# Optimization experiments

Measured on AMD Instinct MI355X. Metric: run time of the kernel, lower is better.

The kernel has to match this reference:

```python
import jax, jax.numpy as jnp
import numpy as np

IN_CH = 1024
ATT_DIM = 1024
B, L1, L2 = 8, 2048, 2048


def setup_inputs() -> dict:
    key = jax.random.key(0)
    ks = jax.random.split(key, 8)
    s = 1.0 / np.sqrt(IN_CH)
    return {
        "input_1": jax.random.normal(ks[0], (B, L1, IN_CH), dtype=jnp.float32),
        "input_2": jax.random.normal(ks[1], (B, L2, IN_CH), dtype=jnp.float32),
        "Wq": jax.random.uniform(ks[2], (IN_CH, ATT_DIM), jnp.float32, -s, s),
        "bq": jnp.zeros((ATT_DIM,), jnp.float32),
        "Wk": jax.random.uniform(ks[3], (IN_CH, ATT_DIM), jnp.float32, -s, s),
        "bk": jnp.zeros((ATT_DIM,), jnp.float32),
        "Wv": jax.random.uniform(ks[4], (IN_CH, ATT_DIM), jnp.float32, -s, s),
        "bv": jnp.zeros((ATT_DIM,), jnp.float32),
    }


def reference(input_1, input_2, Wq, bq, Wk, bk, Wv, bv):
    scale = 1.0 / np.sqrt(ATT_DIM).astype(np.float32)
    Q = jnp.einsum("bld,de->ble", input_1, Wq) + bq  # [B, L1, D]
    K = jnp.einsum("bld,de->ble", input_2, Wk) + bk  # [B, L2, D]
    V = jnp.einsum("bld,de->ble", input_2, Wv) + bv  # [B, L2, D]
    scores = jnp.einsum("bqd,bkd->bqk", Q, K) * scale  # [B, L1, L2]
    scores = jnp.clip(scores, -100.0, 100.0)
    weights = jax.nn.softmax(scores, axis=-1)
    return jnp.einsum("bqk,bkd->bqd", weights, V)  # [B, L1, D]
```

## Files before the change

kernel.cpp:

```cpp
#include <hip/hip_runtime.h>
#include <stdint.h>

typedef __attribute__((ext_vector_type(8))) short bf16x8;
typedef __attribute__((ext_vector_type(4))) float f32x4;
typedef __attribute__((ext_vector_type(4))) unsigned short u16x4;
typedef __attribute__((ext_vector_type(8))) unsigned short u16x8;

__device__ __forceinline__ unsigned short f2bf(float f) {
  unsigned int u = __builtin_bit_cast(unsigned int, f);
  u = (u + 0x7fffu + ((u >> 16) & 1u)) >> 16;
  return (unsigned short)u;
}
__device__ __forceinline__ float bf2f(unsigned short s) {
  unsigned int u = ((unsigned int)s) << 16;
  return __builtin_bit_cast(float, u);
}

__device__ __forceinline__ void g2lds16(const void* g, void* l) {
  __builtin_amdgcn_global_load_lds((const __attribute__((address_space(1))) void*)g,
                                   (__attribute__((address_space(3))) void*)l,
                                   16, 0, 0);
}

__global__ __launch_bounds__(256) void cast_f32_bf16(const float* __restrict__ in0,
                                                     unsigned short* __restrict__ out0,
                                                     const float* __restrict__ in1,
                                                     unsigned short* __restrict__ out1,
                                                     int n4) {
  const float* in = blockIdx.z ? in1 : in0;
  unsigned short* out = blockIdx.z ? out1 : out0;
  int i = blockIdx.x * 256 + threadIdx.x;
  const int stride = gridDim.x * 256;
  for (; i < n4; i += stride) {
    float4 v = reinterpret_cast<const float4*>(in)[i];
    u16x4 o;
    o.x = f2bf(v.x); o.y = f2bf(v.y); o.z = f2bf(v.z); o.w = f2bf(v.w);
    reinterpret_cast<u16x4*>(out)[i] = o;
  }
}

__global__ __launch_bounds__(256) void transpose_cast_w(
    const float* __restrict__ W0, const float* __restrict__ W1, const float* __restrict__ W2,
    unsigned short* __restrict__ T0, unsigned short* __restrict__ T1, unsigned short* __restrict__ T2) {
  const float* W = blockIdx.z == 0 ? W0 : (blockIdx.z == 1 ? W1 : W2);
  unsigned short* T = blockIdx.z == 0 ? T0 : (blockIdx.z == 1 ? T1 : T2);
  __shared__ unsigned short tile[32][33];
  const int tx = threadIdx.x & 31, ty = threadIdx.x >> 5;
  const int r0 = blockIdx.y * 32, c0 = blockIdx.x * 32;
#pragma unroll
  for (int i = 0; i < 4; i++) {
    int r = ty + i * 8;
    tile[r][tx] = f2bf(W[(size_t)(r0 + r) * 1024 + c0 + tx]);
  }
  __syncthreads();
#pragma unroll
  for (int i = 0; i < 4; i++) {
    int r = ty + i * 8;
    T[(size_t)(c0 + r) * 1024 + r0 + tx] = tile[tx][r];
  }
}

#define STAGE(buf, ab, h, kt)                                                          \
  {                                                                                    \
    const char* _s = ((ab) ? Bsrc : Asrc) + (size_t)(h) * 128 * K2 + (size_t)(kt) * 128; \
    char* _d = ldsb + (buf) * 65536 + (ab) * 32768 + (h) * 16384 + tid * 16;           \
    g2lds16(_s, _d);                                                                   \
    g2lds16(_s + 64 * K2, _d + 8192);                                                  \
  }
#define LOADA(buf, mh)                                                                 \
  _Pragma("unroll") for (int mf2 = 0; mf2 < 4; mf2++) {                                \
    const char* _p = ldsb + (buf) * 65536 + arow + ((mh) * 128 + mf2 * 16) * 128;      \
    aA[mf2][0] = *(const bf16x8*)(_p + colk0);                                         \
    aA[mf2][1] = *(const bf16x8*)(_p + colk1);                                         \
  }
#define LOADB(buf, nh)                                                                 \
  _Pragma("unroll") for (int nf2 = 0; nf2 < 2; nf2++) {                                \
    const char* _p = ldsb + (buf) * 65536 + 32768 + brow + ((nh) * 128 + nf2 * 16) * 128; \
    bB[nf2][0] = *(const bf16x8*)(_p + colk0);                                         \
    bB[nf2][1] = *(const bf16x8*)(_p + colk1);                                         \
  }
#define MFMAQ(mh, nh)                                                                  \
  __builtin_amdgcn_s_setprio(1);                                                       \
  _Pragma("unroll") for (int mf2 = 0; mf2 < 4; mf2++)                                  \
      _Pragma("unroll") for (int nf2 = 0; nf2 < 2; nf2++) {                            \
    acc[(mh)*4 + mf2][(nh)*2 + nf2] = __builtin_amdgcn_mfma_f32_16x16x32_bf16(         \
        aA[mf2][0], bB[nf2][0], acc[(mh)*4 + mf2][(nh)*2 + nf2], 0, 0, 0);             \
    acc[(mh)*4 + mf2][(nh)*2 + nf2] = __builtin_amdgcn_mfma_f32_16x16x32_bf16(         \
        aA[mf2][1], bB[nf2][1], acc[(mh)*4 + mf2][(nh)*2 + nf2], 0, 0, 0);             \
  }                                                                                    \
  __builtin_amdgcn_s_setprio(0);
#define BAR() __builtin_amdgcn_s_barrier()
#define VMW(n) asm volatile("s_waitcnt vmcnt(" #n ")" ::: "memory")

template <int MODE>
__global__ __launch_bounds__(512, 2) void gemm256(
    const unsigned short* __restrict__ Aall, const unsigned short* __restrict__ Btall,
    const float* __restrict__ bias, void* __restrict__ Call,
    int gm, int gn, int N, int K, long long sA, long long sB, long long sC, float scale) {
  __shared__ unsigned short lds[2][2][16384];

  const int tid = threadIdx.x;
  const int lane = tid & 63;
  const int w = tid >> 6;
  const int wr = w >> 2, wc = w & 3;
  const int lane16 = lane & 15, kg = lane >> 4;

  const int q8 = gridDim.x >> 3;
  const int swz = (blockIdx.x & 7) * q8 + (blockIdx.x >> 3);
  const int z = swz / (gm * gn);
  const int r2 = swz % (gm * gn);
  const int m0 = (r2 / gn) * 256;
  const int n0 = (r2 % gn) * 256;

  const unsigned short* A = Aall + (size_t)z * sA;
  const unsigned short* Bt = Btall + (size_t)z * sB;
  const size_t K2 = (size_t)K * 2;

  const int rowIn = tid >> 3;
  const int colSw = ((tid & 7) * 16) ^ ((rowIn & 7) << 4);
  const char* Asrc = (const char*)A + (size_t)(m0 + rowIn) * K2 + colSw;
  const char* Bsrc = (const char*)Bt + (size_t)(n0 + rowIn) * K2 + colSw;
  char* ldsb = (char*)&lds[0][0][0];

  const int colk0 = ((kg ^ (lane16 & 7)) << 4);
  const int colk1 = colk0 ^ 64;
  const int arow = (wr * 64 + lane16) * 128;
  const int brow = (wc * 32 + lane16) * 128;

  f32x4 acc[8][4] = {};
  bf16x8 aA[4][2], bB[2][2];

  const int nt = K >> 6;
  const int niter = nt >> 1;

  STAGE(0, 0, 0, 0); STAGE(0, 1, 0, 0); STAGE(0, 0, 1, 0); STAGE(0, 1, 1, 0);
  STAGE(1, 0, 0, 1); STAGE(1, 1, 1, 1);
  VMW(4);
  BAR();

  for (int i = 0; i < niter; i++) {
    const int t = 2 * i;
    const bool more = (i + 1 < niter);
    LOADA(0, 0); LOADB(0, 0);
    STAGE(1, 0, 1, t + 1);
    BAR(); MFMAQ(0, 0); BAR();
    LOADB(0, 1);
    STAGE(1, 1, 0, t + 1);
    BAR(); MFMAQ(0, 1); BAR();
    LOADA(0, 1);
    if (more) STAGE(0, 0, 0, t + 2);
    BAR(); MFMAQ(1, 1); BAR();
    LOADB(0, 0);
    if (more) { STAGE(0, 1, 1, t + 2); VMW(4); } else { VMW(0); }
    BAR(); MFMAQ(1, 0); BAR();
    LOADA(1, 0); LOADB(1, 0);
    if (more) STAGE(0, 0, 1, t + 2);
    BAR(); MFMAQ(0, 0); BAR();
    LOADB(1, 1);
    if (more) STAGE(0, 1, 0, t + 2);
    BAR(); MFMAQ(0, 1); BAR();
    LOADA(1, 1);
    if (more) STAGE(1, 0, 0, t + 3);
    BAR(); MFMAQ(1, 1); BAR();
    LOADB(1, 0);
    if (more) { STAGE(1, 1, 1, t + 3); VMW(4); }
    BAR(); MFMAQ(1, 0); BAR();
  }

  const int rb0 = m0 + wr * 64 + kg * 4;
  const int cb0 = n0 + wc * 32 + lane16;
  if constexpr (MODE == 3) {
    float* C = (float*)Call + (size_t)z * sC;
#pragma unroll
    for (int a = 0; a < 8; a++)
#pragma unroll
      for (int j = 0; j < 4; j++) {
        size_t r = (size_t)(rb0 + (a >> 2) * 128 + (a & 3) * 16 + j);
#pragma unroll
        for (int b = 0; b < 4; b++)
          C[r * N + cb0 + (b >> 1) * 128 + (b & 1) * 16] = acc[a][b][j];
      }
  } else {
    unsigned short* C = (unsigned short*)Call + (size_t)z * sC;
    float cb[4] = {0.f, 0.f, 0.f, 0.f};
    if constexpr (MODE == 0) {
#pragma unroll
      for (int b = 0; b < 4; b++) cb[b] = bias[cb0 + (b >> 1) * 128 + (b & 1) * 16];
    }
#pragma unroll
    for (int a = 0; a < 8; a++)
#pragma unroll
      for (int j = 0; j < 4; j++) {
        int r = rb0 + (a >> 2) * 128 + (a & 3) * 16 + j;
        float rbias = 0.0f;
        if constexpr (MODE == 1) rbias = bias[r];
#pragma unroll
        for (int b = 0; b < 4; b++) {
          float v = acc[a][b][j];
          if constexpr (MODE == 0) v += cb[b];
          if constexpr (MODE == 1) v += rbias;
          if constexpr (MODE == 2) {
            v *= scale;
            v = fminf(fmaxf(v, -100.0f), 100.0f);
          }
          C[(size_t)r * N + cb0 + (b >> 1) * 128 + (b & 1) * 16] = f2bf(v);
        }
      }
  }
}

__global__ __launch_bounds__(256) void softmax_rows(unsigned short* __restrict__ S) {
  const size_t row = blockIdx.x;
  unsigned short* p = S + row * 2048;
  const int tid = threadIdx.x;
  const int lane = tid & 63, wv = tid >> 6;

  u16x8 raw = *reinterpret_cast<const u16x8*>(&p[tid * 8]);
  float v[8];
#pragma unroll
  for (int i = 0; i < 8; i++) v[i] = bf2f(raw[i]);

  float m = v[0];
#pragma unroll
  for (int i = 1; i < 8; i++) m = fmaxf(m, v[i]);
#pragma unroll
  for (int off = 32; off > 0; off >>= 1) m = fmaxf(m, __shfl_xor(m, off));

  __shared__ float red[8];
  if (lane == 0) red[wv] = m;
  __syncthreads();
  m = fmaxf(fmaxf(red[0], red[1]), fmaxf(red[2], red[3]));

  float e[8];
  float s = 0.f;
#pragma unroll
  for (int i = 0; i < 8; i++) { e[i] = __expf(v[i] - m); s += e[i]; }
#pragma unroll
  for (int off = 32; off > 0; off >>= 1) s += __shfl_xor(s, off);
  if (lane == 0) red[4 + wv] = s;
  __syncthreads();
  s = red[4] + red[5] + red[6] + red[7];
  const float inv = 1.0f / s;

  u16x8 o;
#pragma unroll
  for (int i = 0; i < 8; i++) o[i] = f2bf(e[i] * inv);
  *reinterpret_cast<u16x8*>(&p[tid * 8]) = o;
}

extern "C" void kernel_launch(void* const* d_in, const int* in_sizes, int n_in,
                              void* d_out, int out_size, void* d_ws, size_t ws_size,
                              hipStream_t stream) {
  const float* X1 = (const float*)d_in[0];
  const float* X2 = (const float*)d_in[1];
  const float* Wq = (const float*)d_in[2];
  const float* bq = (const float*)d_in[3];
  const float* Wk = (const float*)d_in[4];
  const float* bk = (const float*)d_in[5];
  const float* Wv = (const float*)d_in[6];
  const float* bv = (const float*)d_in[7];

  char* ws = (char*)d_ws;
  const size_t MB = 1024 * 1024;
  unsigned short* X1b = (unsigned short*)(ws);
  unsigned short* X2b = (unsigned short*)(ws + 32 * MB);
  unsigned short* Sbuf = (unsigned short*)(ws);
  unsigned short* Wqt = (unsigned short*)(ws + 64 * MB);
  unsigned short* Wkt = (unsigned short*)(ws + 66 * MB);
  unsigned short* Wvt = (unsigned short*)(ws + 68 * MB);
  unsigned short* Vt = (unsigned short*)(ws + 70 * MB);
  unsigned short* Qb = (unsigned short*)d_out;
  unsigned short* Kb = Qb + 16777216;
  float* out = (float*)d_out;

  cast_f32_bf16<<<dim3(2048, 1, 2), 256, 0, stream>>>(X1, X1b, X2, X2b, 4194304);
  transpose_cast_w<<<dim3(32, 32, 3), 256, 0, stream>>>(Wq, Wk, Wv, Wqt, Wkt, Wvt);

  gemm256<0><<<dim3(256), 512, 0, stream>>>(X1b, Wqt, bq, Qb,
                                            64, 4, 1024, 1024, 0, 0, 0, 1.0f);
  gemm256<0><<<dim3(256), 512, 0, stream>>>(X2b, Wkt, bk, Kb,
                                            64, 4, 1024, 1024, 0, 0, 0, 1.0f);
  gemm256<1><<<dim3(256), 512, 0, stream>>>(Wvt, X2b, bv, Vt,
                                            4, 8, 2048, 1024,
                                            0, 2048LL * 1024, 1024LL * 2048, 1.0f);
  gemm256<2><<<dim3(512), 512, 0, stream>>>(Qb, Kb, nullptr, Sbuf,
                                            8, 8, 2048, 1024,
                                            2048LL * 1024, 2048LL * 1024,
                                            2048LL * 2048, 0.03125f);
  softmax_rows<<<16384, 256, 0, stream>>>(Sbuf);
  gemm256<3><<<dim3(256), 512, 0, stream>>>(Sbuf, Vt, nullptr, out,
                                            8, 4, 1024, 2048,
                                            2048LL * 2048, 1024LL * 2048,
                                            2048LL * 1024, 1.0f);
}
```

Baseline: 438.3 us.

## Stage GEMM epilogue through swizzled LDS for coalesced stores; peel last iteration

The GEMM epilogue now writes accumulator tiles into LDS with an XOR swizzle and then writes them out to global memory as 16-byte row-contiguous vectors, replacing the scattered 2-byte and 4-byte stores. The fp32 output mode goes through LDS in two halves because it needs twice the space. The final main-loop iteration is peeled so the per-stage `more` branches disappear. The MFMA order is also changed to issue all k-slice-0 products before the k-slice-1 ones, which spaces out the dependent accumulator updates. In exchange the epilogue gains extra LDS traffic and barriers.

New measurement: 443.7 us. No clear change (+1.2%).

```diff
diff --git a/kernel.cpp b/kernel.cpp
--- a/kernel.cpp
+++ b/kernel.cpp
@@ -81,12 +81,11 @@
   }
 #define MFMAQ(mh, nh)                                                                  \
   __builtin_amdgcn_s_setprio(1);                                                       \
-  _Pragma("unroll") for (int mf2 = 0; mf2 < 4; mf2++)                                  \
-      _Pragma("unroll") for (int nf2 = 0; nf2 < 2; nf2++) {                            \
+  _Pragma("unroll") for (int ks = 0; ks < 2; ks++)                                     \
+      _Pragma("unroll") for (int mf2 = 0; mf2 < 4; mf2++)                              \
+          _Pragma("unroll") for (int nf2 = 0; nf2 < 2; nf2++) {                        \
     acc[(mh)*4 + mf2][(nh)*2 + nf2] = __builtin_amdgcn_mfma_f32_16x16x32_bf16(         \
-        aA[mf2][0], bB[nf2][0], acc[(mh)*4 + mf2][(nh)*2 + nf2], 0, 0, 0);             \
-    acc[(mh)*4 + mf2][(nh)*2 + nf2] = __builtin_amdgcn_mfma_f32_16x16x32_bf16(         \
-        aA[mf2][1], bB[nf2][1], acc[(mh)*4 + mf2][(nh)*2 + nf2], 0, 0, 0);             \
+        aA[mf2][ks], bB[nf2][ks], acc[(mh)*4 + mf2][(nh)*2 + nf2], 0, 0, 0);           \
   }                                                                                    \
   __builtin_amdgcn_s_setprio(0);
 #define BAR() __builtin_amdgcn_s_barrier()
@@ -138,9 +137,8 @@
   VMW(4);
   BAR();
 
-  for (int i = 0; i < niter; i++) {
+  for (int i = 0; i < niter - 1; i++) {
     const int t = 2 * i;
-    const bool more = (i + 1 < niter);
     LOADA(0, 0); LOADB(0, 0);
     STAGE(1, 0, 1, t + 1);
     BAR(); MFMAQ(0, 0); BAR();
@@ -148,52 +146,62 @@
     STAGE(1, 1, 0, t + 1);
     BAR(); MFMAQ(0, 1); BAR();
     LOADA(0, 1);
-    if (more) STAGE(0, 0, 0, t + 2);
+    STAGE(0, 0, 0, t + 2);
     BAR(); MFMAQ(1, 1); BAR();
     LOADB(0, 0);
-    if (more) { STAGE(0, 1, 1, t + 2); VMW(4); } else { VMW(0); }
+    STAGE(0, 1, 1, t + 2); VMW(4);
     BAR(); MFMAQ(1, 0); BAR();
     LOADA(1, 0); LOADB(1, 0);
-    if (more) STAGE(0, 0, 1, t + 2);
+    STAGE(0, 0, 1, t + 2);
     BAR(); MFMAQ(0, 0); BAR();
     LOADB(1, 1);
-    if (more) STAGE(0, 1, 0, t + 2);
+    STAGE(0, 1, 0, t + 2);
     BAR(); MFMAQ(0, 1); BAR();
     LOADA(1, 1);
-    if (more) STAGE(1, 0, 0, t + 3);
+    STAGE(1, 0, 0, t + 3);
     BAR(); MFMAQ(1, 1); BAR();
     LOADB(1, 0);
-    if (more) { STAGE(1, 1, 1, t + 3); VMW(4); }
+    STAGE(1, 1, 1, t + 3); VMW(4);
     BAR(); MFMAQ(1, 0); BAR();
   }
-
-  const int rb0 = m0 + wr * 64 + kg * 4;
-  const int cb0 = n0 + wc * 32 + lane16;
-  if constexpr (MODE == 3) {
-    float* C = (float*)Call + (size_t)z * sC;
-#pragma unroll
-    for (int a = 0; a < 8; a++)
-#pragma unroll
-      for (int j = 0; j < 4; j++) {
-        size_t r = (size_t)(rb0 + (a >> 2) * 128 + (a & 3) * 16 + j);
-#pragma unroll
-        for (int b = 0; b < 4; b++)
-          C[r * N + cb0 + (b >> 1) * 128 + (b & 1) * 16] = acc[a][b][j];
-      }
-  } else {
+  {
+    const int t = nt - 2;
+    LOADA(0, 0); LOADB(0, 0);
+    STAGE(1, 0, 1, t + 1);
+    BAR(); MFMAQ(0, 0); BAR();
+    LOADB(0, 1);
+    STAGE(1, 1, 0, t + 1);
+    BAR(); MFMAQ(0, 1); BAR();
+    LOADA(0, 1);
+    BAR(); MFMAQ(1, 1); BAR();
+    LOADB(0, 0);
+    VMW(0);
+    BAR(); MFMAQ(1, 0); BAR();
+    LOADA(1, 0); LOADB(1, 0);
+    BAR(); MFMAQ(0, 0); BAR();
+    LOADB(1, 1);
+    BAR(); MFMAQ(0, 1); BAR();
+    LOADA(1, 1);
+    BAR(); MFMAQ(1, 1); BAR();
+    LOADB(1, 0);
+    BAR(); MFMAQ(1, 0); BAR();
+  }
+
+  if constexpr (MODE != 3) {
     unsigned short* C = (unsigned short*)Call + (size_t)z * sC;
     float cb[4] = {0.f, 0.f, 0.f, 0.f};
     if constexpr (MODE == 0) {
 #pragma unroll
-      for (int b = 0; b < 4; b++) cb[b] = bias[cb0 + (b >> 1) * 128 + (b & 1) * 16];
+      for (int b = 0; b < 4; b++)
+        cb[b] = bias[n0 + wc * 32 + lane16 + (b >> 1) * 128 + (b & 1) * 16];
     }
 #pragma unroll
     for (int a = 0; a < 8; a++)
 #pragma unroll
       for (int j = 0; j < 4; j++) {
-        int r = rb0 + (a >> 2) * 128 + (a & 3) * 16 + j;
+        const int rl = (a >> 2) * 128 + wr * 64 + (a & 3) * 16 + kg * 4 + j;
         float rbias = 0.0f;
-        if constexpr (MODE == 1) rbias = bias[r];
+        if constexpr (MODE == 1) rbias = bias[m0 + rl];
 #pragma unroll
         for (int b = 0; b < 4; b++) {
           float v = acc[a][b][j];
@@ -203,9 +211,44 @@
             v *= scale;
             v = fminf(fmaxf(v, -100.0f), 100.0f);
           }
-          C[(size_t)r * N + cb0 + (b >> 1) * 128 + (b & 1) * 16] = f2bf(v);
+          const int cl = (b >> 1) * 128 + wc * 32 + (b & 1) * 16 + lane16;
+          *(unsigned short*)(ldsb + rl * 512 + ((cl * 2) ^ ((rl & 7) << 4))) = f2bf(v);
         }
       }
+    BAR();
+    const int rr = tid >> 5;
+    const int ccb = (tid & 31) * 16;
+#pragma unroll
+    for (int round = 0; round < 16; round++) {
+      const int r = round * 16 + rr;
+      u16x8 val = *(const u16x8*)(ldsb + r * 512 + (ccb ^ ((r & 7) << 4)));
+      *(u16x8*)&C[(size_t)(m0 + r) * N + n0 + (tid & 31) * 8] = val;
+    }
+  } else {
+    float* C = (float*)Call + (size_t)z * sC;
+#pragma unroll
+    for (int half = 0; half < 2; half++) {
+      if (half) BAR();
+#pragma unroll
+      for (int a2 = 0; a2 < 4; a2++)
+#pragma unroll
+        for (int j = 0; j < 4; j++) {
+          const int rl = wr * 64 + a2 * 16 + kg * 4 + j;
+#pragma unroll
+          for (int b = 0; b < 4; b++) {
+            const int cl = (b >> 1) * 128 + wc * 32 + (b & 1) * 16 + lane16;
+            *(float*)(ldsb + rl * 1024 + ((cl * 4) ^ ((rl & 7) << 4))) =
+                acc[half * 4 + a2][b][j];
+          }
+        }
+      BAR();
+#pragma unroll
+      for (int round = 0; round < 16; round++) {
+        const int r = round * 8 + w;
+        f32x4 val = *(const f32x4*)(ldsb + r * 1024 + ((lane * 16) ^ ((r & 7) << 4)));
+        *(f32x4*)&C[(size_t)(m0 + half * 128 + r) * N + n0 + lane * 4] = val;
+      }
+    }
   }
 }
 
```
